# Optimization experiments

Hardware: AMD Instinct MI355X
Metric: run time of the kernel (lower is better)

Reference implementation:

```python
import jax, jax.numpy as jnp
import numpy as np

EMBED_DIM = 512
NUM_HEADS = 8
HEAD_DIM = EMBED_DIM // NUM_HEADS


def setup_inputs() -> dict:
    key = jax.random.key(0)
    ks = jax.random.split(key, 6)
    B, S, D = 2, 4096, EMBED_DIM
    scale = 1.0 / np.sqrt(D)
    inputs = jax.random.normal(ks[0], (B, S, D), dtype=jnp.float32)
    Wq = jax.random.normal(ks[1], (D, D), dtype=jnp.float32) * scale
    Wk = jax.random.normal(ks[2], (D, D), dtype=jnp.float32) * scale
    Wv = jax.random.normal(ks[3], (D, D), dtype=jnp.float32) * scale
    Wo = jax.random.normal(ks[4], (D, D), dtype=jnp.float32) * scale
    zeros = jnp.zeros((D,), dtype=jnp.float32)
    return {"inputs": inputs, "Wq": Wq, "bq": zeros, "Wk": Wk, "bk": zeros,
            "Wv": Wv, "bv": zeros, "Wo": Wo, "bo": zeros}


def _split_heads(x, B, S):
    # [B,S,D] -> [B,H,S,hd]
    return x.reshape(B, S, NUM_HEADS, HEAD_DIM).transpose(0, 2, 1, 3)


def reference(inputs, Wq, bq, Wk, bk, Wv, bv, Wo, bo):
    B, S, D = inputs.shape
    q = _split_heads(inputs @ Wq + bq, B, S)
    k = _split_heads(inputs @ Wk + bk, B, S)
    v = _split_heads(inputs @ Wv + bv, B, S)
    scale = 1.0 / jnp.sqrt(jnp.asarray(HEAD_DIM, dtype=inputs.dtype))
    # full [B,H,S,S] score matrix, as in the original naive SDPA
    scores = jnp.einsum('bhqd,bhkd->bhqk', q, k) * scale
    weights = jax.nn.softmax(scores, axis=-1)
    attn = jnp.einsum('bhqk,bhkd->bhqd', weights, v)
    attn = attn.transpose(0, 2, 1, 3).reshape(B, S, D)
    return attn @ Wo + bo
```

## Files before the change

kernel.cpp:

```cpp
#include <hip/hip_runtime.h>
#include <hip/hip_bf16.h>
#include <stdint.h>


typedef __bf16 bf16x8 __attribute__((ext_vector_type(8)));
typedef float f32x4 __attribute__((ext_vector_type(4)));

using as1_void = __attribute__((address_space(1))) void;
using as3_void = __attribute__((address_space(3))) void;

__device__ __forceinline__ void gload16(const void* g, void* l) {
    __builtin_amdgcn_global_load_lds((const as1_void*)g, (as3_void*)l, 16, 0, 0);
}

__device__ __forceinline__ f32x4 mfma16(bf16x8 a, bf16x8 b, f32x4 c) {
    return __builtin_amdgcn_mfma_f32_16x16x32_bf16(a, b, c, 0, 0, 0);
}

__device__ __forceinline__ uint32_t pkbf(float a, float b) {
    union { __hip_bfloat16 h[2]; uint32_t u; } r;
    r.h[0] = __float2bfloat16(a);
    r.h[1] = __float2bfloat16(b);
    return r.u;
}

__global__ void cvt_all(const float* __restrict__ X, __hip_bfloat16* __restrict__ Xb,
                        const float* __restrict__ w0, const float* __restrict__ w1,
                        const float* __restrict__ w2, const float* __restrict__ w3,
                        __hip_bfloat16* __restrict__ o0, __hip_bfloat16* __restrict__ o1,
                        __hip_bfloat16* __restrict__ o2, __hip_bfloat16* __restrict__ o3) {
    __shared__ float t[32][33];
    const int bid = blockIdx.x, tid = threadIdx.x;
    if (bid < 1024) {
        const float* W; __hip_bfloat16* O;
        switch (bid >> 8) {
            case 0: W = w0; O = o0; break;
            case 1: W = w1; O = o1; break;
            case 2: W = w2; O = o2; break;
            default: W = w3; O = o3; break;
        }
        int rem = bid & 255;
        int n0 = (rem & 15) * 32, k0 = (rem >> 4) * 32;
        int tx = tid & 31, ty = tid >> 5;
        for (int j = 0; j < 4; ++j)
            t[ty + 8 * j][tx] = W[(size_t)(k0 + ty + 8 * j) * 512 + n0 + tx];
        __syncthreads();
        for (int j = 0; j < 4; ++j)
            O[(size_t)(n0 + ty + 8 * j) * 512 + k0 + tx] = __float2bfloat16(t[tx][ty + 8 * j]);
    } else {
        int i = ((bid - 1024) * 256 + tid) * 4;
        float4 v = *reinterpret_cast<const float4*>(X + i);
        uint2 u;
        u.x = pkbf(v.x, v.y);
        u.y = pkbf(v.z, v.w);
        *reinterpret_cast<uint2*>(Xb + i) = u;
    }
}

__global__ __launch_bounds__(256, 2) void gemm_qkv(
    const __hip_bfloat16* __restrict__ A, const __hip_bfloat16* __restrict__ Bt,
    const float* __restrict__ bq, const float* __restrict__ bk, const float* __restrict__ bv,
    __hip_bfloat16* __restrict__ Qb, __hip_bfloat16* __restrict__ Kb,
    __hip_bfloat16* __restrict__ Vtb, float qs)
{
    const int K = 512;
    __shared__ __hip_bfloat16 Abuf[128 * 32];
    __shared__ __hip_bfloat16 Bbuf[128 * 32];
    const int tid = threadIdx.x, w = tid >> 6, lane = tid & 63;
    const int col = lane & 15, quad = lane >> 4;
    const int wr = w >> 1, wc = w & 1;
    const int tileN = blockIdx.x * 128, tileM = blockIdx.y * 128;

    f32x4 acc[4][4] = {};

    for (int k0 = 0; k0 < K; k0 += 32) {
        for (int i = 0; i < 2; ++i) {
            int g = w * 2 + i;
            int chunk = g * 64 + lane;
            int row = chunk >> 2, c8 = chunk & 3;
            gload16(A + (size_t)(tileM + row) * K + k0 + c8 * 8, Abuf + g * 512);
            gload16(Bt + (size_t)(tileN + row) * K + k0 + c8 * 8, Bbuf + g * 512);
        }
        __syncthreads();
        bf16x8 af[4], bfr[4];
        for (int mt = 0; mt < 4; ++mt)
            af[mt] = *reinterpret_cast<const bf16x8*>(Abuf + (wr * 64 + mt * 16 + col) * 32 + quad * 8);
        for (int nt = 0; nt < 4; ++nt)
            bfr[nt] = *reinterpret_cast<const bf16x8*>(Bbuf + (wc * 64 + nt * 16 + col) * 32 + quad * 8);
        for (int mt = 0; mt < 4; ++mt)
            for (int nt = 0; nt < 4; ++nt)
                acc[mt][nt] = mfma16(af[mt], bfr[nt], acc[mt][nt]);
        __syncthreads();
    }

    const int seg = (tileN + wc * 64) >> 9;
    const float* bias = (seg == 0) ? bq : (seg == 1) ? bk : bv;
    const float scale = (seg == 0) ? qs : 1.0f;
    __hip_bfloat16* outp = (seg == 0) ? Qb : (seg == 1) ? Kb : Vtb;

    for (int mt = 0; mt < 4; ++mt) {
        for (int nt = 0; nt < 4; ++nt) {
            int n = tileN + wc * 64 + nt * 16 + col;
            int nn = n & 511, h = nn >> 6, d = nn & 63;
            float bn = bias[nn];
            for (int r = 0; r < 4; ++r) {
                int m = tileM + wr * 64 + mt * 16 + quad * 4 + r;
                int b = m >> 12, s = m & 4095;
                float v = (acc[mt][nt][r] + bn) * scale;
                size_t off;
                if (seg < 2) off = (((size_t)(b * 8 + h) * 4096 + s) << 6) + d;
                else         off = (((size_t)(b * 8 + h) * 64 + d) << 12) + s;
                outp[off] = __float2bfloat16(v);
            }
        }
    }
}

__global__ __launch_bounds__(256, 2) void gemm_out(
    const __hip_bfloat16* __restrict__ A, const __hip_bfloat16* __restrict__ Bt,
    const float* __restrict__ bias, float* __restrict__ out)
{
    const int N = 512, K = 512;
    __shared__ __hip_bfloat16 Abuf[128 * 32];
    __shared__ __hip_bfloat16 Bbuf[64 * 32];
    const int tid = threadIdx.x, w = tid >> 6, lane = tid & 63;
    const int col = lane & 15, quad = lane >> 4;
    const int tileN = blockIdx.x * 64, tileM = blockIdx.y * 128;

    f32x4 acc[2][4] = {};

    for (int k0 = 0; k0 < K; k0 += 32) {
        for (int i = 0; i < 2; ++i) {
            int g = w * 2 + i;
            int chunk = g * 64 + lane;
            int row = chunk >> 2, c8 = chunk & 3;
            gload16(A + (size_t)(tileM + row) * K + k0 + c8 * 8, Abuf + g * 512);
        }
        {
            int row = tid >> 2, c8 = tid & 3;
            gload16(Bt + (size_t)(tileN + row) * K + k0 + c8 * 8, Bbuf + tid * 8);
        }
        __syncthreads();
        bf16x8 af[2], bfr[4];
        for (int mt = 0; mt < 2; ++mt)
            af[mt] = *reinterpret_cast<const bf16x8*>(Abuf + (w * 32 + mt * 16 + col) * 32 + quad * 8);
        for (int nt = 0; nt < 4; ++nt)
            bfr[nt] = *reinterpret_cast<const bf16x8*>(Bbuf + (nt * 16 + col) * 32 + quad * 8);
        for (int mt = 0; mt < 2; ++mt)
            for (int nt = 0; nt < 4; ++nt)
                acc[mt][nt] = mfma16(af[mt], bfr[nt], acc[mt][nt]);
        __syncthreads();
    }

    for (int mt = 0; mt < 2; ++mt) {
        for (int nt = 0; nt < 4; ++nt) {
            int n = tileN + nt * 16 + col;
            float bn = bias[n];
            for (int r = 0; r < 4; ++r) {
                int m = tileM + w * 32 + mt * 16 + quad * 4 + r;
                out[(size_t)m * N + n] = acc[mt][nt][r] + bn;
            }
        }
    }
}

__global__ __launch_bounds__(256) void flash(
    const __hip_bfloat16* __restrict__ Q,
    const __hip_bfloat16* __restrict__ Kq,
    const __hip_bfloat16* __restrict__ Vt,
    __hip_bfloat16* __restrict__ attnb)
{
    __shared__ __hip_bfloat16 KT[2][4096];
    __shared__ __hip_bfloat16 VB[2][4096];
    __shared__ uint32_t TB[4][1024];

    const int bh = blockIdx.y, b = bh >> 3, h = bh & 7;
    const int tid = threadIdx.x, w = tid >> 6, lane = tid & 63;
    const int col = lane & 15, quad = lane >> 4;
    const int q0 = blockIdx.x * 128 + w * 32;
    const int c7 = col & 7;

    const __hip_bfloat16* Qh = Q + (size_t)bh * 4096 * 64;
    const __hip_bfloat16* Kh = Kq + (size_t)bh * 4096 * 64;
    const __hip_bfloat16* Vh = Vt + (size_t)bh * 64 * 4096;

    bf16x8 aq[2][2];
    for (int qh = 0; qh < 2; ++qh)
        for (int ks = 0; ks < 2; ++ks)
            aq[qh][ks] = *reinterpret_cast<const bf16x8*>(
                Qh + (size_t)(q0 + qh * 16 + col) * 64 + ks * 32 + quad * 8);

    const __hip_bfloat16* ksrc[2];
    const __hip_bfloat16* vsrc[2];
    int ldsoff[2];
    for (int i = 0; i < 2; ++i) {
        int c = i * 256 + tid;
        int row = c >> 3, s8 = (c & 7) ^ (row & 7);
        ksrc[i] = Kh + row * 64 + s8 * 8;
        vsrc[i] = Vh + (size_t)row * 4096 + s8 * 8;
        ldsoff[i] = (i * 256 + w * 64) * 8;
    }

    bf16x8 ones;
    for (int j = 0; j < 8; ++j) ones[j] = (__bf16)1.0f;

    f32x4 o[4][2] = {};
    f32x4 accl[2] = {};
    f32x4 sc[2][4][2];

    uint32_t* TBw = &TB[w][0];
    uint2* TBw2 = reinterpret_cast<uint2*>(TBw);

    gload16(ksrc[0], &KT[0][ldsoff[0]]);
    gload16(ksrc[1], &KT[0][ldsoff[1]]);
    gload16(vsrc[0], &VB[0][ldsoff[0]]);
    gload16(vsrc[1], &VB[0][ldsoff[1]]);
    gload16(ksrc[0] + 4096, &KT[1][ldsoff[0]]);
    gload16(ksrc[1] + 4096, &KT[1][ldsoff[1]]);
    __syncthreads();

    for (int kg = 0; kg < 4; ++kg)
        for (int qh = 0; qh < 2; ++qh)
            sc[0][kg][qh] = (f32x4){0.f, 0.f, 0.f, 0.f};
    for (int ks = 0; ks < 2; ++ks)
        for (int kg = 0; kg < 4; ++kg) {
            bf16x8 ak = *reinterpret_cast<const bf16x8*>(
                &KT[0][(kg * 16 + col) * 64 + (((ks * 4 + quad) ^ c7) << 3)]);
            for (int qh = 0; qh < 2; ++qh)
                sc[0][kg][qh] = mfma16(ak, aq[qh][ks], sc[0][kg][qh]);
        }
    __syncthreads();

#define FLASH_BODY(KT_, P_)                                                     \
    {                                                                           \
        const int kt_ = (KT_);                                                  \
        int kk = kt_ + 2; if (kk > 63) kk = 63;                                 \
        gload16(ksrc[0] + (size_t)kk * 4096, &KT[(P_)][ldsoff[0]]);             \
        gload16(ksrc[1] + (size_t)kk * 4096, &KT[(P_)][ldsoff[1]]);             \
        gload16(vsrc[0] + (size_t)(kt_ + 1) * 64, &VB[1 - (P_)][ldsoff[0]]);    \
        gload16(vsrc[1] + (size_t)(kt_ + 1) * 64, &VB[1 - (P_)][ldsoff[1]]);    \
        for (int kg = 0; kg < 4; ++kg)                                          \
            for (int qh = 0; qh < 2; ++qh) {                                    \
                f32x4 v = sc[(P_)][kg][qh];                                     \
                uint2 u;                                                        \
                u.x = pkbf(__builtin_amdgcn_exp2f(v[0]),                        \
                           __builtin_amdgcn_exp2f(v[1]));                       \
                u.y = pkbf(__builtin_amdgcn_exp2f(v[2]),                        \
                           __builtin_amdgcn_exp2f(v[3]));                       \
                TBw2[(qh * 16 + col) * 16 +                                     \
                     (((kg * 2 + (quad >> 1)) ^ c7) << 1) + (quad & 1)] = u;    \
            }                                                                   \
        for (int kg = 0; kg < 4; ++kg)                                          \
            for (int qh = 0; qh < 2; ++qh)                                      \
                sc[1 - (P_)][kg][qh] = (f32x4){0.f, 0.f, 0.f, 0.f};             \
        for (int ks = 0; ks < 2; ++ks)                                          \
            for (int kg = 0; kg < 4; ++kg) {                                    \
                bf16x8 ak = *reinterpret_cast<const bf16x8*>(                   \
                    &KT[1 - (P_)][(kg * 16 + col) * 64 +                        \
                                  (((ks * 4 + quad) ^ c7) << 3)]);              \
                for (int qh = 0; qh < 2; ++qh)                                  \
                    sc[1 - (P_)][kg][qh] =                                      \
                        mfma16(ak, aq[qh][ks], sc[1 - (P_)][kg][qh]);           \
            }                                                                   \
        bf16x8 bp[2][2];                                                        \
        for (int qh = 0; qh < 2; ++qh)                                          \
            for (int ks = 0; ks < 2; ++ks)                                      \
                bp[qh][ks] = *reinterpret_cast<const bf16x8*>(                  \
                    &TBw[(qh * 16 + col) * 32 + (((ks * 4 + quad) ^ c7) << 2)]);\
        for (int ks = 0; ks < 2; ++ks) {                                        \
            for (int dt = 0; dt < 4; ++dt) {                                    \
                bf16x8 av = *reinterpret_cast<const bf16x8*>(                   \
                    &VB[(P_)][(dt * 16 + col) * 64 +                            \
                              (((ks * 4 + quad) ^ c7) << 3)]);                  \
                for (int qh = 0; qh < 2; ++qh)                                  \
                    o[dt][qh] = mfma16(av, bp[qh][ks], o[dt][qh]);              \
            }                                                                   \
            accl[0] = mfma16(ones, bp[0][ks], accl[0]);                         \
            accl[1] = mfma16(ones, bp[1][ks], accl[1]);                         \
        }                                                                       \
        __syncthreads();                                                        \
    }

    FLASH_BODY(0, 0)
    for (int kth = 0; kth < 31; ++kth) {
        FLASH_BODY(2 * kth + 1, 1)
        FLASH_BODY(2 * kth + 2, 0)
    }
    {
        for (int kg = 0; kg < 4; ++kg)
            for (int qh = 0; qh < 2; ++qh) {
                f32x4 v = sc[1][kg][qh];
                uint2 u;
                u.x = pkbf(__builtin_amdgcn_exp2f(v[0]), __builtin_amdgcn_exp2f(v[1]));
                u.y = pkbf(__builtin_amdgcn_exp2f(v[2]), __builtin_amdgcn_exp2f(v[3]));
                TBw2[(qh * 16 + col) * 16 + (((kg * 2 + (quad >> 1)) ^ c7) << 1) + (quad & 1)] = u;
            }
        bf16x8 bp[2][2];
        for (int qh = 0; qh < 2; ++qh)
            for (int ks = 0; ks < 2; ++ks)
                bp[qh][ks] = *reinterpret_cast<const bf16x8*>(
                    &TBw[(qh * 16 + col) * 32 + (((ks * 4 + quad) ^ c7) << 2)]);
        for (int ks = 0; ks < 2; ++ks) {
            for (int dt = 0; dt < 4; ++dt) {
                bf16x8 av = *reinterpret_cast<const bf16x8*>(
                    &VB[1][(dt * 16 + col) * 64 + (((ks * 4 + quad) ^ c7) << 3)]);
                for (int qh = 0; qh < 2; ++qh)
                    o[dt][qh] = mfma16(av, bp[qh][ks], o[dt][qh]);
            }
            accl[0] = mfma16(ones, bp[0][ks], accl[0]);
            accl[1] = mfma16(ones, bp[1][ks], accl[1]);
        }
    }
#undef FLASH_BODY

    for (int qh = 0; qh < 2; ++qh) {
        float inv = 1.0f / accl[qh][0];
        int s = q0 + qh * 16 + col;
        __hip_bfloat16* dst = attnb + ((size_t)b * 4096 + s) * 512 + h * 64 + quad * 4;
        for (int dt = 0; dt < 4; ++dt) {
            uint2 u;
            u.x = pkbf(o[dt][qh][0] * inv, o[dt][qh][1] * inv);
            u.y = pkbf(o[dt][qh][2] * inv, o[dt][qh][3] * inv);
            *reinterpret_cast<uint2*>(dst + dt * 16) = u;
        }
    }
}

extern "C" void kernel_launch(void* const* d_in, const int* in_sizes, int n_in,
                              void* d_out, int out_size, void* d_ws, size_t ws_size,
                              hipStream_t stream) {
    const float* X  = (const float*)d_in[0];
    const float* Wq = (const float*)d_in[1];
    const float* bq = (const float*)d_in[2];
    const float* Wk = (const float*)d_in[3];
    const float* bk = (const float*)d_in[4];
    const float* Wv = (const float*)d_in[5];
    const float* bv = (const float*)d_in[6];
    const float* Wo = (const float*)d_in[7];
    const float* bo = (const float*)d_in[8];
    float* out = (float*)d_out;

    char* ws = (char*)d_ws;
    __hip_bfloat16* Xb  = (__hip_bfloat16*)(ws);
    __hip_bfloat16* Wqt = (__hip_bfloat16*)(ws + ((size_t)8 << 20));
    __hip_bfloat16* Wkt = Wqt + 512 * 512;
    __hip_bfloat16* Wvt = Wkt + 512 * 512;
    __hip_bfloat16* Wot = Wvt + 512 * 512;
    __hip_bfloat16* Qb  = (__hip_bfloat16*)(ws + ((size_t)10 << 20));
    __hip_bfloat16* Kb  = (__hip_bfloat16*)(ws + ((size_t)18 << 20));
    __hip_bfloat16* Vtb = (__hip_bfloat16*)(ws + ((size_t)26 << 20));
    __hip_bfloat16* Atb = (__hip_bfloat16*)(ws + ((size_t)34 << 20));

    cvt_all<<<5120, 256, 0, stream>>>(X, Xb, Wq, Wk, Wv, Wo, Wqt, Wkt, Wvt, Wot);

    const float qs = 0.125f * 1.4426950408889634f;
    gemm_qkv<<<dim3(12, 64), 256, 0, stream>>>(Xb, Wqt, bq, bk, bv, Qb, Kb, Vtb, qs);
    flash<<<dim3(32, 16), 256, 0, stream>>>(Qb, Kb, Vtb, Atb);
    gemm_out<<<dim3(8, 64), 256, 0, stream>>>(Atb, Wot, bo, out);
}
```

Measured before the change: 214.6 us.

## Split attention keys across two blocks and merge partial outputs

The flash kernel becomes a split-K version. Each block handles half of the key/value sequence, which doubles the grid to 1024 blocks so more of the CUs are filled. Each block writes unnormalized fp16 partial outputs and partial row sums, both scaled down to avoid overflow, and a new merge kernel adds the halves, normalizes, and writes bf16 in the head-interleaved layout. The per-iteration body is also simplified: QK scores are no longer software-pipelined one tile ahead, and the LDS buffer for probabilities is smaller, aimed at higher occupancy under launch_bounds(256,4). The cost is an extra kernel launch, extra global traffic for the partials, and precision risk from the fp16 intermediates.

New measurement: 215.3 us. Within noise of the previous version (+0.3%).

```diff
diff --git a/kernel.cpp b/kernel.cpp
--- a/kernel.cpp
+++ b/kernel.cpp
@@ -1,5 +1,6 @@
 #include <hip/hip_runtime.h>
 #include <hip/hip_bf16.h>
+#include <hip/hip_fp16.h>
 #include <stdint.h>
 
 
@@ -21,6 +22,13 @@
     union { __hip_bfloat16 h[2]; uint32_t u; } r;
     r.h[0] = __float2bfloat16(a);
     r.h[1] = __float2bfloat16(b);
+    return r.u;
+}
+
+__device__ __forceinline__ uint32_t pkhalf(float a, float b) {
+    union { __half h[2]; uint32_t u; } r;
+    r.h[0] = __float2half(a);
+    r.h[1] = __float2half(b);
     return r.u;
 }
 
@@ -164,166 +172,164 @@
     }
 }
 
-__global__ __launch_bounds__(256) void flash(
+__global__ __launch_bounds__(256, 4) void flash_part(
     const __hip_bfloat16* __restrict__ Q,
     const __hip_bfloat16* __restrict__ Kq,
     const __hip_bfloat16* __restrict__ Vt,
-    __hip_bfloat16* __restrict__ attnb)
+    __half* __restrict__ O0, __half* __restrict__ O1,
+    float* __restrict__ Lp)
 {
     __shared__ __hip_bfloat16 KT[2][4096];
     __shared__ __hip_bfloat16 VB[2][4096];
-    __shared__ uint32_t TB[4][1024];
-
-    const int bh = blockIdx.y, b = bh >> 3, h = bh & 7;
+    __shared__ uint32_t TB[4][512];
+
+    const int bh = blockIdx.y, ks = blockIdx.z;
     const int tid = threadIdx.x, w = tid >> 6, lane = tid & 63;
     const int col = lane & 15, quad = lane >> 4;
     const int q0 = blockIdx.x * 128 + w * 32;
     const int c7 = col & 7;
 
     const __hip_bfloat16* Qh = Q + (size_t)bh * 4096 * 64;
-    const __hip_bfloat16* Kh = Kq + (size_t)bh * 4096 * 64;
-    const __hip_bfloat16* Vh = Vt + (size_t)bh * 64 * 4096;
+    const __hip_bfloat16* Kh = Kq + (size_t)bh * 4096 * 64 + (size_t)ks * 2048 * 64;
+    const __hip_bfloat16* Vh = Vt + (size_t)bh * 64 * 4096 + (size_t)ks * 2048;
 
     bf16x8 aq[2][2];
     for (int qh = 0; qh < 2; ++qh)
-        for (int ks = 0; ks < 2; ++ks)
-            aq[qh][ks] = *reinterpret_cast<const bf16x8*>(
-                Qh + (size_t)(q0 + qh * 16 + col) * 64 + ks * 32 + quad * 8);
-
-    const __hip_bfloat16* ksrc[2];
-    const __hip_bfloat16* vsrc[2];
+        for (int k2 = 0; k2 < 2; ++k2)
+            aq[qh][k2] = *reinterpret_cast<const bf16x8*>(
+                Qh + (size_t)(q0 + qh * 16 + col) * 64 + k2 * 32 + quad * 8);
+
+    const __hip_bfloat16 *ksrc0, *vsrc0;
     int ldsoff[2];
-    for (int i = 0; i < 2; ++i) {
-        int c = i * 256 + tid;
-        int row = c >> 3, s8 = (c & 7) ^ (row & 7);
-        ksrc[i] = Kh + row * 64 + s8 * 8;
-        vsrc[i] = Vh + (size_t)row * 4096 + s8 * 8;
-        ldsoff[i] = (i * 256 + w * 64) * 8;
-    }
+    {
+        int row = tid >> 3, s8 = (tid & 7) ^ (row & 7);
+        ksrc0 = Kh + row * 64 + s8 * 8;
+        vsrc0 = Vh + (size_t)row * 4096 + s8 * 8;
+        ldsoff[0] = (w * 64) * 8;
+        ldsoff[1] = (256 + w * 64) * 8;
+    }
+    const __hip_bfloat16* ksrc1 = ksrc0 + 32 * 64;
+    const __hip_bfloat16* vsrc1 = vsrc0 + (size_t)32 * 4096;
 
     bf16x8 ones;
     for (int j = 0; j < 8; ++j) ones[j] = (__bf16)1.0f;
 
     f32x4 o[4][2] = {};
     f32x4 accl[2] = {};
-    f32x4 sc[2][4][2];
+    f32x4 sc[4][2];
+    const f32x4 z4 = {0.f, 0.f, 0.f, 0.f};
 
     uint32_t* TBw = &TB[w][0];
     uint2* TBw2 = reinterpret_cast<uint2*>(TBw);
 
-    gload16(ksrc[0], &KT[0][ldsoff[0]]);
-    gload16(ksrc[1], &KT[0][ldsoff[1]]);
-    gload16(vsrc[0], &VB[0][ldsoff[0]]);
-    gload16(vsrc[1], &VB[0][ldsoff[1]]);
-    gload16(ksrc[0] + 4096, &KT[1][ldsoff[0]]);
-    gload16(ksrc[1] + 4096, &KT[1][ldsoff[1]]);
+    gload16(ksrc0, &KT[0][ldsoff[0]]);
+    gload16(ksrc1, &KT[0][ldsoff[1]]);
+    gload16(vsrc0, &VB[0][ldsoff[0]]);
+    gload16(vsrc1, &VB[0][ldsoff[1]]);
     __syncthreads();
 
-    for (int kg = 0; kg < 4; ++kg)
-        for (int qh = 0; qh < 2; ++qh)
-            sc[0][kg][qh] = (f32x4){0.f, 0.f, 0.f, 0.f};
-    for (int ks = 0; ks < 2; ++ks)
-        for (int kg = 0; kg < 4; ++kg) {
-            bf16x8 ak = *reinterpret_cast<const bf16x8*>(
-                &KT[0][(kg * 16 + col) * 64 + (((ks * 4 + quad) ^ c7) << 3)]);
-            for (int qh = 0; qh < 2; ++qh)
-                sc[0][kg][qh] = mfma16(ak, aq[qh][ks], sc[0][kg][qh]);
-        }
-    __syncthreads();
-
-#define FLASH_BODY(KT_, P_)                                                     \
+#define BODY(KT_, P_)                                                           \
     {                                                                           \
-        const int kt_ = (KT_);                                                  \
-        int kk = kt_ + 2; if (kk > 63) kk = 63;                                 \
-        gload16(ksrc[0] + (size_t)kk * 4096, &KT[(P_)][ldsoff[0]]);             \
-        gload16(ksrc[1] + (size_t)kk * 4096, &KT[(P_)][ldsoff[1]]);             \
-        gload16(vsrc[0] + (size_t)(kt_ + 1) * 64, &VB[1 - (P_)][ldsoff[0]]);    \
-        gload16(vsrc[1] + (size_t)(kt_ + 1) * 64, &VB[1 - (P_)][ldsoff[1]]);    \
-        for (int kg = 0; kg < 4; ++kg)                                          \
-            for (int qh = 0; qh < 2; ++qh) {                                    \
-                f32x4 v = sc[(P_)][kg][qh];                                     \
+        int kk = (KT_) + 1; if (kk > 31) kk = 31;   \
+        gload16(ksrc0 + (size_t)kk * 4096, &KT[1 - (P_)][ldsoff[0]]);           \
+        gload16(ksrc1 + (size_t)kk * 4096, &KT[1 - (P_)][ldsoff[1]]);           \
+        gload16(vsrc0 + (size_t)kk * 64, &VB[1 - (P_)][ldsoff[0]]);             \
+        gload16(vsrc1 + (size_t)kk * 64, &VB[1 - (P_)][ldsoff[1]]);             \
+                                                      \
+        for (int kg = 0; kg < 4; ++kg) {                                        \
+            bf16x8 ak = *reinterpret_cast<const bf16x8*>(                       \
+                &KT[(P_)][(kg * 16 + col) * 64 + ((quad ^ c7) << 3)]);          \
+            for (int qh = 0; qh < 2; ++qh)                                      \
+                sc[kg][qh] = mfma16(ak, aq[qh][0], z4);                         \
+        }                                                                       \
+        for (int kg = 0; kg < 4; ++kg) {                                        \
+            bf16x8 ak = *reinterpret_cast<const bf16x8*>(                       \
+                &KT[(P_)][(kg * 16 + col) * 64 + (((4 + quad) ^ c7) << 3)]);    \
+            for (int qh = 0; qh < 2; ++qh)                                      \
+                sc[kg][qh] = mfma16(ak, aq[qh][1], sc[kg][qh]);                 \
+        }                                                                       \
+                        \
+        bf16x8 bp[2][2];                                                        \
+        for (int qh = 0; qh < 2; ++qh) {                                        \
+            for (int kg = 0; kg < 4; ++kg) {                                    \
+                f32x4 v = sc[kg][qh];                                           \
                 uint2 u;                                                        \
                 u.x = pkbf(__builtin_amdgcn_exp2f(v[0]),                        \
                            __builtin_amdgcn_exp2f(v[1]));                       \
                 u.y = pkbf(__builtin_amdgcn_exp2f(v[2]),                        \
                            __builtin_amdgcn_exp2f(v[3]));                       \
-                TBw2[(qh * 16 + col) * 16 +                                     \
-                     (((kg * 2 + (quad >> 1)) ^ c7) << 1) + (quad & 1)] = u;    \
+                TBw2[col * 16 + (((kg * 2 + (quad >> 1)) ^ c7) << 1) +          \
+                     (quad & 1)] = u;                                           \
             }                                                                   \
-        for (int kg = 0; kg < 4; ++kg)                                          \
-            for (int qh = 0; qh < 2; ++qh)                                      \
-                sc[1 - (P_)][kg][qh] = (f32x4){0.f, 0.f, 0.f, 0.f};             \
-        for (int ks = 0; ks < 2; ++ks)                                          \
-            for (int kg = 0; kg < 4; ++kg) {                                    \
-                bf16x8 ak = *reinterpret_cast<const bf16x8*>(                   \
-                    &KT[1 - (P_)][(kg * 16 + col) * 64 +                        \
-                                  (((ks * 4 + quad) ^ c7) << 3)]);              \
-                for (int qh = 0; qh < 2; ++qh)                                  \
-                    sc[1 - (P_)][kg][qh] =                                      \
-                        mfma16(ak, aq[qh][ks], sc[1 - (P_)][kg][qh]);           \
-            }                                                                   \
-        bf16x8 bp[2][2];                                                        \
-        for (int qh = 0; qh < 2; ++qh)                                          \
-            for (int ks = 0; ks < 2; ++ks)                                      \
-                bp[qh][ks] = *reinterpret_cast<const bf16x8*>(                  \
-                    &TBw[(qh * 16 + col) * 32 + (((ks * 4 + quad) ^ c7) << 2)]);\
-        for (int ks = 0; ks < 2; ++ks) {                                        \
+            bp[qh][0] = *reinterpret_cast<const bf16x8*>(                       \
+                &TBw[col * 32 + ((quad ^ c7) << 2)]);                           \
+            bp[qh][1] = *reinterpret_cast<const bf16x8*>(                       \
+                &TBw[col * 32 + (((4 + quad) ^ c7) << 2)]);                     \
+        }                                                                       \
+                                                     \
+        for (int k2 = 0; k2 < 2; ++k2) {                                        \
             for (int dt = 0; dt < 4; ++dt) {                                    \
                 bf16x8 av = *reinterpret_cast<const bf16x8*>(                   \
                     &VB[(P_)][(dt * 16 + col) * 64 +                            \
-                              (((ks * 4 + quad) ^ c7) << 3)]);                  \
+                              (((k2 * 4 + quad) ^ c7) << 3)]);                  \
                 for (int qh = 0; qh < 2; ++qh)                                  \
-                    o[dt][qh] = mfma16(av, bp[qh][ks], o[dt][qh]);              \
+                    o[dt][qh] = mfma16(av, bp[qh][k2], o[dt][qh]);              \
             }                                                                   \
-            accl[0] = mfma16(ones, bp[0][ks], accl[0]);                         \
-            accl[1] = mfma16(ones, bp[1][ks], accl[1]);                         \
+            accl[0] = mfma16(ones, bp[0][k2], accl[0]);                         \
+            accl[1] = mfma16(ones, bp[1][k2], accl[1]);                         \
         }                                                                       \
         __syncthreads();                                                        \
     }
 
-    FLASH_BODY(0, 0)
-    for (int kth = 0; kth < 31; ++kth) {
-        FLASH_BODY(2 * kth + 1, 1)
-        FLASH_BODY(2 * kth + 2, 0)
-    }
-    {
-        for (int kg = 0; kg < 4; ++kg)
-            for (int qh = 0; qh < 2; ++qh) {
-                f32x4 v = sc[1][kg][qh];
-                uint2 u;
-                u.x = pkbf(__builtin_amdgcn_exp2f(v[0]), __builtin_amdgcn_exp2f(v[1]));
-                u.y = pkbf(__builtin_amdgcn_exp2f(v[2]), __builtin_amdgcn_exp2f(v[3]));
-                TBw2[(qh * 16 + col) * 16 + (((kg * 2 + (quad >> 1)) ^ c7) << 1) + (quad & 1)] = u;
-            }
-        bf16x8 bp[2][2];
-        for (int qh = 0; qh < 2; ++qh)
-            for (int ks = 0; ks < 2; ++ks)
-                bp[qh][ks] = *reinterpret_cast<const bf16x8*>(
-                    &TBw[(qh * 16 + col) * 32 + (((ks * 4 + quad) ^ c7) << 2)]);
-        for (int ks = 0; ks < 2; ++ks) {
-            for (int dt = 0; dt < 4; ++dt) {
-                bf16x8 av = *reinterpret_cast<const bf16x8*>(
-                    &VB[1][(dt * 16 + col) * 64 + (((ks * 4 + quad) ^ c7) << 3)]);
-                for (int qh = 0; qh < 2; ++qh)
-                    o[dt][qh] = mfma16(av, bp[qh][ks], o[dt][qh]);
-            }
-            accl[0] = mfma16(ones, bp[0][ks], accl[0]);
-            accl[1] = mfma16(ones, bp[1][ks], accl[1]);
-        }
-    }
-#undef FLASH_BODY
-
+    BODY(0, 0)
+    for (int kth = 0; kth < 15; ++kth) {
+        BODY(2 * kth + 1, 1)
+        BODY(2 * kth + 2, 0)
+    }
+    BODY(31, 1)
+#undef BODY
+
+    __half* Op = (ks == 0 ? O0 : O1) + ((size_t)bh * 4096) * 64;
     for (int qh = 0; qh < 2; ++qh) {
-        float inv = 1.0f / accl[qh][0];
-        int s = q0 + qh * 16 + col;
-        __hip_bfloat16* dst = attnb + ((size_t)b * 4096 + s) * 512 + h * 64 + quad * 4;
+        int q = q0 + qh * 16 + col;
+        __half* dst = Op + (size_t)q * 64 + quad * 4;
         for (int dt = 0; dt < 4; ++dt) {
+            f32x4 v = o[dt][qh] * 0.0625f;
             uint2 u;
-            u.x = pkbf(o[dt][qh][0] * inv, o[dt][qh][1] * inv);
-            u.y = pkbf(o[dt][qh][2] * inv, o[dt][qh][3] * inv);
+            u.x = pkhalf(v[0], v[1]);
+            u.y = pkhalf(v[2], v[3]);
             *reinterpret_cast<uint2*>(dst + dt * 16) = u;
         }
     }
+    if (quad == 0) {
+        float* lq = Lp + (size_t)ks * 65536 + bh * 4096 + q0;
+        lq[col] = accl[0][0] * 0.0625f;
+        lq[16 + col] = accl[1][0] * 0.0625f;
+    }
+}
+
+__global__ void merge(const __half* __restrict__ O0, const __half* __restrict__ O1,
+                      const float* __restrict__ Lp, __hip_bfloat16* __restrict__ Atb)
+{
+    int i4 = (blockIdx.x * 256 + threadIdx.x) * 4;
+    uint2 a = *reinterpret_cast<const uint2*>(O0 + i4);
+    uint2 b = *reinterpret_cast<const uint2*>(O1 + i4);
+    int j = i4 >> 6;
+    float inv = 1.0f / (Lp[j] + Lp[65536 + j]);
+    union { uint32_t u; __half h[2]; } ax, ay, bx, by;
+    ax.u = a.x; ay.u = a.y; bx.u = b.x; by.u = b.y;
+    float s0 = (__half2float(ax.h[0]) + __half2float(bx.h[0])) * inv;
+    float s1 = (__half2float(ax.h[1]) + __half2float(bx.h[1])) * inv;
+    float s2 = (__half2float(ay.h[0]) + __half2float(by.h[0])) * inv;
+    float s3 = (__half2float(ay.h[1]) + __half2float(by.h[1])) * inv;
+    uint2 r;
+    r.x = pkbf(s0, s1);
+    r.y = pkbf(s2, s3);
+    int bh = i4 >> 18;
+    int rem = i4 & ((1 << 18) - 1);
+    int q = rem >> 6, d = rem & 63;
+    size_t off = ((size_t)(bh >> 3) * 4096 + q) * 512 + (bh & 7) * 64 + d;
+    *reinterpret_cast<uint2*>(Atb + off) = r;
 }
 
 extern "C" void kernel_launch(void* const* d_in, const int* in_sizes, int n_in,
@@ -349,12 +355,16 @@
     __hip_bfloat16* Qb  = (__hip_bfloat16*)(ws + ((size_t)10 << 20));
     __hip_bfloat16* Kb  = (__hip_bfloat16*)(ws + ((size_t)18 << 20));
     __hip_bfloat16* Vtb = (__hip_bfloat16*)(ws + ((size_t)26 << 20));
-    __hip_bfloat16* Atb = (__hip_bfloat16*)(ws + ((size_t)34 << 20));
+    __half* O0 = (__half*)(ws);
+    float*  Lp = (float*)(ws + ((size_t)8 << 20));
+    __half* O1 = (__half*)(ws + ((size_t)34 << 20));
+    __hip_bfloat16* Atb = (__hip_bfloat16*)(ws + ((size_t)10 << 20));
 
     cvt_all<<<5120, 256, 0, stream>>>(X, Xb, Wq, Wk, Wv, Wo, Wqt, Wkt, Wvt, Wot);
 
     const float qs = 0.125f * 1.4426950408889634f;
     gemm_qkv<<<dim3(12, 64), 256, 0, stream>>>(Xb, Wqt, bq, bk, bv, Qb, Kb, Vtb, qs);
-    flash<<<dim3(32, 16), 256, 0, stream>>>(Qb, Kb, Vtb, Atb);
+    flash_part<<<dim3(32, 16, 2), 256, 0, stream>>>(Qb, Kb, Vtb, O0, O1, Lp);
+    merge<<<4096, 256, 0, stream>>>(O0, O1, Lp, Atb);
     gemm_out<<<dim3(8, 64), 256, 0, stream>>>(Atb, Wot, bo, out);
 }
```
